# Kernel tuning notes

Hardware: AMD Instinct MI355X
Metric: run time of the kernel (lower is better)

## Reference

```python
import jax, jax.numpy as jnp
import numpy as np

B, L, G = 8192, 4096, 512  # batch, n_fine_labels, meta_label_size
META_PARAM = 1.0           # config['meta_param']
LOG_CLAMP = -100.0         # torch BCELoss clamps log terms at -100


def setup_inputs() -> dict:
    key = jax.random.key(0)
    k1, k2 = jax.random.split(key)
    logits = jax.random.normal(k1, (B, L), dtype=jnp.float32)
    true_y = (jax.random.uniform(k2, (B, L)) < 0.02).astype(jnp.float32)
    # label -> meta-group id; arange % G ensures every group is non-empty
    group_ids = (jnp.arange(L) % G).astype(jnp.int32)
    return {"logits": logits, "true_y": true_y, "group_ids": group_ids}


def reference(logits, true_y, group_ids):
    # y_hat = sigmoid(logits); per-group prod(1 - y_hat) done in log space:
    # log(1 - sigmoid(x)) = log_sigmoid(-x)
    log1m = jax.nn.log_sigmoid(-logits)  # [B, L]
    # segment-sum of logs over the label dim == log of ragged group product
    log_meta = jax.ops.segment_sum(log1m.T, group_ids, num_segments=G).T  # [B, G]
    meta_probs = jnp.exp(log_meta)  # [B, G], prod_{l in group g} (1 - y_hat[b, l])

    # meta_y[b, g] = 1 if any true fine label in group g (generate_meta_y)
    meta_y = (jax.ops.segment_sum(true_y.T, group_ids, num_segments=G).T > 0)
    meta_y = meta_y.astype(logits.dtype)

    # BCELoss(meta_probs, meta_y), mean reduction, log terms clamped at -100
    log_p = jnp.maximum(log_meta, LOG_CLAMP)
    log_1mp = jnp.maximum(jnp.log1p(-meta_probs), LOG_CLAMP)
    bce = -jnp.mean(meta_y * log_p + (1.0 - meta_y) * log_1mp)
    return bce * META_PARAM
```

## Files before the change

kernel.cpp:

```cpp
#include <hip/hip_runtime.h>
#include <math.h>

#define LDIM  4096
#define GDIM  512
#define TPB   256
#define ROWS_PER_BLOCK 2
#define LOG_CLAMP_F (-100.0f)

typedef float f32x4 __attribute__((ext_vector_type(4)));

__device__ __forceinline__ float neg_softplus(float x) {
    const float e = __expf(-fabsf(x));
    return -(fmaxf(x, 0.0f) + __logf(1.0f + e));
}

__device__ __forceinline__ float bce_term(float lm, float flag) {
    const float p   = __expf(lm);
    const float pos = fmaxf(lm, LOG_CLAMP_F);
    const float neg = fmaxf(log1pf(-p), LOG_CLAMP_F);
    return (flag > 0.0f) ? pos : neg;
}

__device__ __forceinline__ f32x4 nt_load4(const float* p) {
    return __builtin_nontemporal_load((const f32x4*)p);
}

__global__ __launch_bounds__(TPB) void meta_row_kernel(
    const float* __restrict__ logits,
    const float* __restrict__ true_y,
    float*       __restrict__ partial)
{
    const int t = threadIdx.x;
    const int u = t & 127;
    const int r = blockIdx.x * ROWS_PER_BLOCK + (t >> 7);

    const float* xr = logits + (size_t)r * LDIM;
    const float* yr = true_y + (size_t)r * LDIM;

    f32x4 xs[8], ys[8];
#pragma unroll
    for (int j = 0; j < 8; ++j) {
        xs[j] = nt_load4(xr + 4 * (u + 128 * j));
        ys[j] = nt_load4(yr + 4 * (u + 128 * j));
    }
    __builtin_amdgcn_sched_barrier(0);

    float lm0 = 0.f, lm1 = 0.f, lm2 = 0.f, lm3 = 0.f;
    float f0 = 0.f, f1 = 0.f, f2 = 0.f, f3 = 0.f;
#pragma unroll
    for (int j = 0; j < 8; ++j) {
        lm0 += neg_softplus(xs[j].x);
        lm1 += neg_softplus(xs[j].y);
        lm2 += neg_softplus(xs[j].z);
        lm3 += neg_softplus(xs[j].w);
        f0 = fmaxf(f0, ys[j].x);
        f1 = fmaxf(f1, ys[j].y);
        f2 = fmaxf(f2, ys[j].z);
        f3 = fmaxf(f3, ys[j].w);
    }

    float total = bce_term(lm0, f0) + bce_term(lm1, f1)
                + bce_term(lm2, f2) + bce_term(lm3, f3);

    __shared__ float s_red[TPB / 64];
#pragma unroll
    for (int off = 32; off > 0; off >>= 1)
        total += __shfl_down(total, off, 64);
    const int lane = t & 63, wid = t >> 6;
    if (lane == 0) s_red[wid] = total;
    __syncthreads();
    if (t == 0) {
        float s = 0.0f;
#pragma unroll
        for (int w = 0; w < TPB / 64; ++w) s += s_red[w];
        partial[blockIdx.x] = s;
    }
}

__global__ __launch_bounds__(256) void meta_final_kernel(
    const float* __restrict__ partial, int n4, double inv_count,
    float* __restrict__ out)
{
    const int t = threadIdx.x;
    double s = 0.0;
    const float4* p4 = (const float4*)partial;
    for (int i = t; i < n4; i += 256) {
        const float4 v = p4[i];
        s += (double)v.x + (double)v.y + (double)v.z + (double)v.w;
    }
#pragma unroll
    for (int off = 32; off > 0; off >>= 1)
        s += __shfl_down(s, off, 64);
    __shared__ double sr[4];
    if ((t & 63) == 0) sr[t >> 6] = s;
    __syncthreads();
    if (t == 0) {
        double tot = sr[0] + sr[1] + sr[2] + sr[3];
        out[0] = (float)(-tot * inv_count);
    }
}

extern "C" void kernel_launch(void* const* d_in, const int* in_sizes, int n_in,
                              void* d_out, int out_size, void* d_ws, size_t ws_size,
                              hipStream_t stream) {
    const float* logits = (const float*)d_in[0];
    const float* true_y = (const float*)d_in[1];
    float*       out    = (float*)d_out;

    const int Ldim = in_sizes[2];
    const int B    = in_sizes[0] / Ldim;
    const int nblocks = B / ROWS_PER_BLOCK;
    float* partial = (float*)d_ws;

    meta_row_kernel<<<nblocks, TPB, 0, stream>>>(logits, true_y, partial);

    const double inv_count = 1.0 / ((double)B * (double)GDIM);
    meta_final_kernel<<<1, 256, 0, stream>>>(partial, nblocks / 4, inv_count, out);
}
```

Baseline: 252.7 us.

## Use persistent grid with double-buffered register prefetch of row pairs

Replaces the one-block-per-row-pair launch with a fixed grid of 512 persistent blocks that stride over row pairs. Each block loads the next pair into a second register buffer while computing on the current one, so loads overlap with the softplus math. Per-thread accumulation moves to double, and there are now 512 double partials. This doubles register use per thread and reduces the number of resident waves, which could hurt latency hiding.

```diff
diff --git a/kernel.cpp b/kernel.cpp
--- a/kernel.cpp
+++ b/kernel.cpp
@@ -4,7 +4,7 @@
 #define LDIM  4096
 #define GDIM  512
 #define TPB   256
-#define ROWS_PER_BLOCK 2
+#define NBLK  512
 #define LOG_CLAMP_F (-100.0f)
 
 typedef float f32x4 __attribute__((ext_vector_type(4)));
@@ -25,26 +25,22 @@
     return __builtin_nontemporal_load((const f32x4*)p);
 }
 
-__global__ __launch_bounds__(TPB) void meta_row_kernel(
-    const float* __restrict__ logits,
-    const float* __restrict__ true_y,
-    float*       __restrict__ partial)
-{
-    const int t = threadIdx.x;
-    const int u = t & 127;
-    const int r = blockIdx.x * ROWS_PER_BLOCK + (t >> 7);
-
+__device__ __forceinline__ void load_rp(const float* __restrict__ logits,
+                                        const float* __restrict__ true_y,
+                                        int rp, int u, int half,
+                                        f32x4 (&xs)[8], f32x4 (&ys)[8]) {
+    const int r = rp * 2 + half;
     const float* xr = logits + (size_t)r * LDIM;
     const float* yr = true_y + (size_t)r * LDIM;
-
-    f32x4 xs[8], ys[8];
 #pragma unroll
     for (int j = 0; j < 8; ++j) {
         xs[j] = nt_load4(xr + 4 * (u + 128 * j));
         ys[j] = nt_load4(yr + 4 * (u + 128 * j));
     }
-    __builtin_amdgcn_sched_barrier(0);
+}
 
+__device__ __forceinline__ double compute_rp(const f32x4 (&xs)[8],
+                                             const f32x4 (&ys)[8]) {
     float lm0 = 0.f, lm1 = 0.f, lm2 = 0.f, lm3 = 0.f;
     float f0 = 0.f, f1 = 0.f, f2 = 0.f, f3 = 0.f;
 #pragma unroll
@@ -58,19 +54,53 @@
         f2 = fmaxf(f2, ys[j].z);
         f3 = fmaxf(f3, ys[j].w);
     }
+    return (double)bce_term(lm0, f0) + (double)bce_term(lm1, f1)
+         + (double)bce_term(lm2, f2) + (double)bce_term(lm3, f3);
+}
 
-    float total = bce_term(lm0, f0) + bce_term(lm1, f1)
-                + bce_term(lm2, f2) + bce_term(lm3, f3);
+__global__ __launch_bounds__(TPB, 2) void meta_row_kernel(
+    const float* __restrict__ logits,
+    const float* __restrict__ true_y,
+    double*      __restrict__ partial,
+    int rp_total)
+{
+    const int t    = threadIdx.x;
+    const int u    = t & 127;
+    const int half = t >> 7;
 
-    __shared__ float s_red[TPB / 64];
+    f32x4 xa[8], ya[8], xb[8], yb[8];
+    double acc = 0.0;
+
+    int rp0 = blockIdx.x;
+    if (rp0 < rp_total) {
+        load_rp(logits, true_y, rp0, u, half, xa, ya);
+        for (;;) {
+            const int rp1 = rp0 + NBLK;
+            const bool h1 = rp1 < rp_total;
+            if (h1) load_rp(logits, true_y, rp1, u, half, xb, yb);
+            __builtin_amdgcn_sched_barrier(0);
+            acc += compute_rp(xa, ya);
+            if (!h1) break;
+
+            const int rp2 = rp1 + NBLK;
+            const bool h2 = rp2 < rp_total;
+            if (h2) load_rp(logits, true_y, rp2, u, half, xa, ya);
+            __builtin_amdgcn_sched_barrier(0);
+            acc += compute_rp(xb, yb);
+            if (!h2) break;
+            rp0 = rp2;
+        }
+    }
+
+    __shared__ double s_red[TPB / 64];
 #pragma unroll
     for (int off = 32; off > 0; off >>= 1)
-        total += __shfl_down(total, off, 64);
+        acc += __shfl_down(acc, off, 64);
     const int lane = t & 63, wid = t >> 6;
-    if (lane == 0) s_red[wid] = total;
+    if (lane == 0) s_red[wid] = acc;
     __syncthreads();
     if (t == 0) {
-        float s = 0.0f;
+        double s = 0.0;
 #pragma unroll
         for (int w = 0; w < TPB / 64; ++w) s += s_red[w];
         partial[blockIdx.x] = s;
@@ -78,16 +108,12 @@
 }
 
 __global__ __launch_bounds__(256) void meta_final_kernel(
-    const float* __restrict__ partial, int n4, double inv_count,
+    const double* __restrict__ partial, int n, double inv_count,
     float* __restrict__ out)
 {
     const int t = threadIdx.x;
     double s = 0.0;
-    const float4* p4 = (const float4*)partial;
-    for (int i = t; i < n4; i += 256) {
-        const float4 v = p4[i];
-        s += (double)v.x + (double)v.y + (double)v.z + (double)v.w;
-    }
+    for (int i = t; i < n; i += 256) s += partial[i];
 #pragma unroll
     for (int off = 32; off > 0; off >>= 1)
         s += __shfl_down(s, off, 64);
@@ -107,13 +133,13 @@
     const float* true_y = (const float*)d_in[1];
     float*       out    = (float*)d_out;
 
-    const int Ldim = in_sizes[2];
-    const int B    = in_sizes[0] / Ldim;
-    const int nblocks = B / ROWS_PER_BLOCK;
-    float* partial = (float*)d_ws;
+    const int Ldim     = in_sizes[2];
+    const int B        = in_sizes[0] / Ldim;
+    const int rp_total = B / 2;
+    double* partial = (double*)d_ws;
 
-    meta_row_kernel<<<nblocks, TPB, 0, stream>>>(logits, true_y, partial);
+    meta_row_kernel<<<NBLK, TPB, 0, stream>>>(logits, true_y, partial, rp_total);
 
     const double inv_count = 1.0 / ((double)B * (double)GDIM);
-    meta_final_kernel<<<1, 256, 0, stream>>>(partial, nblocks / 4, inv_count, out);
+    meta_final_kernel<<<1, 256, 0, stream>>>(partial, NBLK, inv_count, out);
 }
```

Result: slower. 260.5 us (+3.1%).
